# Kernel tuning notes

Measured on AMD Instinct MI355X. Metric: run time of the kernel, lower is better.

Reference implementation:

```python
import jax, jax.numpy as jnp
import numpy as np

EPS = 1e-06

def setup_inputs() -> dict:
    key = jax.random.key(0)
    k1, k2, k3, k4, k5 = jax.random.split(key, 5)
    B, T, D, Dv = 4, 2048, 128, 128
    q = jax.random.normal(k1, (B, T, D), dtype=jnp.float32)
    k = jax.random.normal(k2, (B, T, D), dtype=jnp.float32)
    v = jax.random.normal(k3, (B, T, Dv), dtype=jnp.float32)
    # phi = nn.Linear(dim, dim) followed by ELU; torch Linear default init ~ U(-1/sqrt(D), 1/sqrt(D))
    lim = 1.0 / np.sqrt(D)
    W_phi = jax.random.uniform(k4, (D, D), minval=-lim, maxval=lim, dtype=jnp.float32)
    b_phi = jax.random.uniform(k5, (D,), minval=-lim, maxval=lim, dtype=jnp.float32)
    return {"q": q, "k": k, "v": v, "W_phi": W_phi, "b_phi": b_phi}

def reference(q, k, v, W_phi, b_phi):
    # feature map: phi(x) = ELU(x @ W^T + b) + 1  (positive features)
    def phi(x):
        return jax.nn.elu(jnp.einsum('btd,ed->bte', x, W_phi) + b_phi) + 1.0

    Q = phi(q)                      # [B,T,D]
    K = phi(k)                      # [B,T,D]
    # causal recurrent state (zero initial state since h=None):
    # z_t = sum_{tau<=t} K_tau                 -> [B,T,D]
    # s_t = sum_{tau<=t} K_tau (outer) v_tau   -> [B,T,D,Dv]
    z = jnp.cumsum(K, axis=1)
    s = jnp.cumsum(K[..., :, None] * v[..., None, :], axis=1)
    den = jnp.einsum('btd,btd->bt', Q, z) + EPS          # [B,T]
    out = jnp.einsum('btd,btde->bte', Q, s) / den[..., None]  # [B,T,Dv]
    return out
```

## Files before the change

### kernel.cpp

```cpp
#include <hip/hip_runtime.h>
#include <hip/hip_bf16.h>

#define BB 4
#define TT 2048
#define DD 128
#define CHK 64
#define NCHK 32
#define NCHKS (BB*NCHK)

typedef __attribute__((ext_vector_type(8))) short  bf16x8;
typedef __attribute__((ext_vector_type(4))) float  f32x4;

#define MFMA(a,b,c) __builtin_amdgcn_mfma_f32_16x16x32_bf16(a, b, c, 0, 0, 0)

__device__ __forceinline__ short f2b(float f) {
    union { float f; unsigned u; } x; x.f = f;
    unsigned r = x.u + 0x7fffu + ((x.u >> 16) & 1u);
    return (short)(r >> 16);
}
__device__ __forceinline__ float b2f(short s) {
    union { unsigned u; float f; } x; x.u = ((unsigned)(unsigned short)s) << 16;
    return x.f;
}
__device__ __forceinline__ bf16x8 cvt8(const float* p) {
    float4 a = *(const float4*)p, b = *(const float4*)(p + 4);
    bf16x8 r;
    r[0]=f2b(a.x); r[1]=f2b(a.y); r[2]=f2b(a.z); r[3]=f2b(a.w);
    r[4]=f2b(b.x); r[5]=f2b(b.y); r[6]=f2b(b.z); r[7]=f2b(b.w);
    return r;
}

__device__ __forceinline__ void w_to_lds(const float* __restrict__ W,
                                         short (*Wl)[DD + 8], int tid) {
    #pragma unroll
    for (int it = 0; it < 16; ++it) {
        int i = tid + it * 256;
        int row = i >> 5, c4 = (i & 31) * 4;
        float4 v = *(const float4*)(W + (size_t)row * DD + c4);
        unsigned lo = (unsigned short)f2b(v.x) | ((unsigned)(unsigned short)f2b(v.y) << 16);
        unsigned hi = (unsigned short)f2b(v.z) | ((unsigned)(unsigned short)f2b(v.w) << 16);
        uint2 p; p.x = lo; p.y = hi;
        *(uint2*)&Wl[row][c4] = p;
    }
}

__global__ __launch_bounds__(256) void k1_chunk(const float* __restrict__ kin,
                                                const float* __restrict__ vin,
                                                const float* __restrict__ W,
                                                const float* __restrict__ bias,
                                                short* __restrict__ Ss_g,
                                                float* __restrict__ zc_g,
                                                short* __restrict__ vT_g,
                                                short* __restrict__ Kf_g) {
    int c = blockIdx.x >> 1, h = blockIdx.x & 1;
    const float* kc = kin + (size_t)c * CHK * DD;
    const float* vc = vin + (size_t)c * CHK * DD;

    __shared__ __align__(16) short Wl  [DD][DD + 8];
    __shared__ __align__(16) short KfT [DD][CHK + 8];
    __shared__ __align__(16) short vT  [CHK][CHK + 8];
    __shared__ __align__(16) short stage[CHK][DD + 8];

    int tid = threadIdx.x, lane = tid & 63, w = tid >> 6;
    int l15 = lane & 15, l4 = lane >> 4;
    const f32x4 z4 = {0.f, 0.f, 0.f, 0.f};

    bf16x8 afk[4];
    {
        int row = 16 * w + l15;
        #pragma unroll
        for (int kk = 0; kk < 4; ++kk) afk[kk] = cvt8(kc + row * DD + kk * 32 + l4 * 8);
    }
    w_to_lds(W, Wl, tid);
    #pragma unroll
    for (int it = 0; it < 4; ++it) {
        int i = tid + it * 256;
        int t = i >> 4, c4 = (i & 15) * 4;
        float4 vv = *(const float4*)(vc + t * DD + 64 * h + c4);
        vT[c4 + 0][t] = f2b(vv.x); vT[c4 + 1][t] = f2b(vv.y);
        vT[c4 + 2][t] = f2b(vv.z); vT[c4 + 3][t] = f2b(vv.w);
    }
    __syncthreads();

    #pragma unroll
    for (int n = 0; n < 8; ++n) {
        int e = 16 * n + l15;
        f32x4 d = z4;
        #pragma unroll
        for (int kk = 0; kk < 4; ++kk) {
            bf16x8 bw = *(const bf16x8*)&Wl[e][kk * 32 + l4 * 8];
            d = MFMA(afk[kk], bw, d);
        }
        float bv = bias[e];
        #pragma unroll
        for (int j = 0; j < 4; ++j) {
            float zv = d[j] + bv;
            short r = f2b((zv > 0.f) ? (zv + 1.f) : __expf(zv));
            int t = 16 * w + l4 * 4 + j;
            KfT[e][t] = r;
            if (h == 0) stage[t][e] = r;
        }
    }
    __syncthreads();

    if (h == 0) {
        short* dst = Kf_g + (size_t)c * CHK * DD;
        #pragma unroll
        for (int it = 0; it < 4; ++it) {
            int i = tid + it * 256;
            int t = i >> 4, u = (i & 15) * 8;
            *(bf16x8*)(dst + t * DD + u) = *(const bf16x8*)&stage[t][u];
        }
        if (tid < DD) {
            float s = 0.f;
            #pragma unroll
            for (int t8 = 0; t8 < CHK / 8; ++t8) {
                bf16x8 kv = *(const bf16x8*)&KfT[tid][t8 * 8];
                #pragma unroll
                for (int j = 0; j < 8; ++j) s += b2f(kv[j]);
            }
            zc_g[(size_t)c * DD + tid] = s;
        }
    }
    #pragma unroll
    for (int it = 0; it < 2; ++it) {
        int i = tid + it * 256;
        int e = i >> 3, t0 = (i & 7) * 8;
        *(bf16x8*)(vT_g + (size_t)c * DD * CHK + (64 * h + e) * CHK + t0) =
            *(const bf16x8*)&vT[e][t0];
    }

    f32x4 sacc[2][4];
    #pragma unroll
    for (int mi = 0; mi < 2; ++mi)
        #pragma unroll
        for (int n = 0; n < 4; ++n) sacc[mi][n] = z4;
    #pragma unroll
    for (int kk = 0; kk < 2; ++kk) {
        bf16x8 afr[2];
        #pragma unroll
        for (int mi = 0; mi < 2; ++mi)
            afr[mi] = *(const bf16x8*)&KfT[16 * (2 * w + mi) + l15][kk * 32 + l4 * 8];
        #pragma unroll
        for (int n = 0; n < 4; ++n) {
            bf16x8 bfr = *(const bf16x8*)&vT[16 * n + l15][kk * 32 + l4 * 8];
            sacc[0][n] = MFMA(afr[0], bfr, sacc[0][n]);
            sacc[1][n] = MFMA(afr[1], bfr, sacc[1][n]);
        }
    }
    __syncthreads();

    #pragma unroll
    for (int mi = 0; mi < 2; ++mi)
        #pragma unroll
        for (int n = 0; n < 4; ++n) {
            int e = 16 * n + l15;
            #pragma unroll
            for (int j = 0; j < 4; ++j)
                stage[e][16 * (2 * w + mi) + l4 * 4 + j] = f2b(sacc[mi][n][j]);
        }
    __syncthreads();

    short* dst = Ss_g + (size_t)c * DD * DD + (size_t)(64 * h) * DD;
    #pragma unroll
    for (int it = 0; it < 4; ++it) {
        int i = tid + it * 256;
        int e = i >> 4, u = (i & 15) * 8;
        *(bf16x8*)(dst + e * DD + u) = *(const bf16x8*)&stage[e][u];
    }
}

__global__ __launch_bounds__(128) void k2_scan(const short* __restrict__ Ss_g,
                                               const float* __restrict__ zc_g,
                                               short* __restrict__ Sp_g,
                                               float* __restrict__ zp_g) {
    int e = blockIdx.x & 127, b = blockIdx.x >> 7;
    int d = threadIdx.x;
    size_t base = ((size_t)(b * NCHK) * DD + e) * DD + d;
    const size_t stride = (size_t)DD * DD;

    float vals[NCHK];
    #pragma unroll
    for (int c2 = 0; c2 < NCHK; ++c2) vals[c2] = b2f(Ss_g[base + c2 * stride]);
    float run = 0.f;
    #pragma unroll
    for (int c2 = 0; c2 < NCHK; ++c2) {
        Sp_g[base + c2 * stride] = f2b(run);
        run += vals[c2];
    }
    if (e == 0) {
        float vz[NCHK];
        #pragma unroll
        for (int c2 = 0; c2 < NCHK; ++c2) vz[c2] = zc_g[(size_t)(b * NCHK + c2) * DD + d];
        float rz = 0.f;
        #pragma unroll
        for (int c2 = 0; c2 < NCHK; ++c2) {
            zp_g[(size_t)(b * NCHK + c2) * DD + d] = rz;
            rz += vz[c2];
        }
    }
}

__global__ __launch_bounds__(256) void k3_out(const float* __restrict__ q,
                                              const float* __restrict__ W,
                                              const float* __restrict__ bias,
                                              const short* __restrict__ Kf_g,
                                              const short* __restrict__ Sp_g,
                                              const float* __restrict__ zp_g,
                                              const short* __restrict__ vT_g,
                                              float* __restrict__ out) {
    int c = blockIdx.x >> 1, h = blockIdx.x & 1;

    __shared__ __align__(16) short Wl[DD][DD + 8];
    __shared__ __align__(16) short Qf[CHK][DD + 8];
    __shared__ __align__(16) short Kf[CHK][DD + 8];
    __shared__ __align__(16) short Ps[CHK][CHK + 8];
    __shared__ float zs[DD];
    __shared__ float den[CHK];

    int tid = threadIdx.x, lane = tid & 63, w = tid >> 6;
    int l15 = lane & 15, l4 = lane >> 4;
    const f32x4 z4 = {0.f, 0.f, 0.f, 0.f};

    if (tid < DD) zs[tid] = zp_g[(size_t)c * DD + tid];

    const float* qc = q + (size_t)c * CHK * DD;
    bf16x8 afq[4];
    {
        int row = 16 * w + l15;
        #pragma unroll
        for (int kk = 0; kk < 4; ++kk)
            afq[kk] = cvt8(qc + row * DD + kk * 32 + l4 * 8);
    }
    w_to_lds(W, Wl, tid);
    {
        const short* src = Kf_g + (size_t)c * CHK * DD;
        #pragma unroll
        for (int it = 0; it < 4; ++it) {
            int i = tid + it * 256;
            int t = i >> 4, u = (i & 15) * 8;
            *(bf16x8*)&Kf[t][u] = *(const bf16x8*)(src + t * DD + u);
        }
    }
    __syncthreads();

    #pragma unroll
    for (int n = 0; n < 8; ++n) {
        int e = 16 * n + l15;
        f32x4 dq = z4;
        #pragma unroll
        for (int kk = 0; kk < 4; ++kk) {
            bf16x8 bw = *(const bf16x8*)&Wl[e][kk * 32 + l4 * 8];
            dq = MFMA(afq[kk], bw, dq);
        }
        float bv = bias[e];
        #pragma unroll
        for (int j = 0; j < 4; ++j) {
            float zq = dq[j] + bv;
            Qf[16 * w + l4 * 4 + j][e] = f2b((zq > 0.f) ? (zq + 1.f) : __expf(zq));
        }
    }
    __syncthreads();

    bf16x8 aq[4];
    #pragma unroll
    for (int kk = 0; kk < 4; ++kk)
        aq[kk] = *(const bf16x8*)&Qf[16 * w + l15][kk * 32 + l4 * 8];
    #pragma unroll
    for (int n2 = 0; n2 < 4; ++n2) {
        f32x4 p = z4;
        #pragma unroll
        for (int kk = 0; kk < 4; ++kk) {
            bf16x8 bk = *(const bf16x8*)&Kf[16 * n2 + l15][kk * 32 + l4 * 8];
            p = MFMA(aq[kk], bk, p);
        }
        int t2 = 16 * n2 + l15;
        #pragma unroll
        for (int j = 0; j < 4; ++j) {
            int t = 16 * w + l4 * 4 + j;
            Ps[t][t2] = (t2 <= t) ? f2b(p[j]) : (short)0;
        }
    }
    __syncthreads();

    if (tid < CHK) {
        float s = 1e-6f;
        #pragma unroll
        for (int t8 = 0; t8 < CHK / 8; ++t8) {
            bf16x8 pv = *(const bf16x8*)&Ps[tid][t8 * 8];
            #pragma unroll
            for (int j = 0; j < 8; ++j) s += b2f(pv[j]);
        }
        #pragma unroll
        for (int d8 = 0; d8 < DD / 8; ++d8) {
            bf16x8 qv = *(const bf16x8*)&Qf[tid][d8 * 8];
            #pragma unroll
            for (int j = 0; j < 8; ++j) s += b2f(qv[j]) * zs[d8 * 8 + j];
        }
        den[tid] = s;
    }

    bf16x8 ap[2];
    #pragma unroll
    for (int kk = 0; kk < 2; ++kk)
        ap[kk] = *(const bf16x8*)&Ps[16 * w + l15][kk * 32 + l4 * 8];

    const short* Sp  = Sp_g + (size_t)c * DD * DD;
    const short* vTg = vT_g + (size_t)c * DD * CHK;
    f32x4 oacc[4];
    #pragma unroll
    for (int n = 0; n < 4; ++n) oacc[n] = z4;
    #pragma unroll
    for (int n = 0; n < 4; ++n) {
        int e = 64 * h + 16 * n + l15;
        #pragma unroll
        for (int kk = 0; kk < 4; ++kk) {
            bf16x8 bs = *(const bf16x8*)(Sp + e * DD + kk * 32 + l4 * 8);
            oacc[n] = MFMA(aq[kk], bs, oacc[n]);
        }
        #pragma unroll
        for (int kk = 0; kk < 2; ++kk) {
            bf16x8 bv = *(const bf16x8*)(vTg + e * CHK + kk * 32 + l4 * 8);
            oacc[n] = MFMA(ap[kk], bv, oacc[n]);
        }
    }
    __syncthreads();

    float* oc = out + (size_t)c * CHK * DD;
    float invs[4];
    #pragma unroll
    for (int j = 0; j < 4; ++j) invs[j] = 1.0f / den[16 * w + l4 * 4 + j];
    #pragma unroll
    for (int n = 0; n < 4; ++n) {
        int e = 64 * h + 16 * n + l15;
        #pragma unroll
        for (int j = 0; j < 4; ++j) {
            int t = 16 * w + l4 * 4 + j;
            oc[t * DD + e] = oacc[n][j] * invs[j];
        }
    }
}

extern "C" void kernel_launch(void* const* d_in, const int* in_sizes, int n_in,
                              void* d_out, int out_size, void* d_ws, size_t ws_size,
                              hipStream_t stream) {
    const float* q  = (const float*)d_in[0];
    const float* k  = (const float*)d_in[1];
    const float* v  = (const float*)d_in[2];
    const float* W  = (const float*)d_in[3];
    const float* bi = (const float*)d_in[4];
    float* out = (float*)d_out;

    float* zc_g = (float*)d_ws;
    float* zp_g = zc_g + (size_t)NCHKS * DD;
    short* Ss_g = (short*)(zp_g + (size_t)NCHKS * DD);
    short* Sp_g = Ss_g + (size_t)NCHKS * DD * DD;
    short* vT_g = Sp_g + (size_t)NCHKS * DD * DD;
    short* Kf_g = vT_g + (size_t)NCHKS * DD * CHK;

    k1_chunk<<<2 * NCHKS, 256, 0, stream>>>(k, v, W, bi, Ss_g, zc_g, vT_g, Kf_g);
    k2_scan<<<512, 128, 0, stream>>>(Ss_g, zc_g, Sp_g, zp_g);
    k3_out<<<2 * NCHKS, 256, 0, stream>>>(q, W, bi, Kf_g, Sp_g, zp_g, vT_g, out);
}
```

Measured before the change: 28.38 us.

## Compute Q feature map in chunk kernel and pass bf16 Qf to output kernel

Moves the phi(q) projection out of the output kernel into the first chunk kernel, where the h=1 block (previously idle for the feature store) computes Q features and writes them as bf16 to workspace. The output kernel then just loads precomputed Qf and Kf from global memory instead of reloading W into LDS and running its own projection. This cuts duplicated W staging across both h-halves in k3 and shrinks k3's LDS footprint. In exchange it adds an extra bf16 global write and read of Q features and more work for the h=1 blocks of k1.

After: 27.31 us. -3.8%, faster.

```diff
diff --git a/kernel.cpp b/kernel.cpp
--- a/kernel.cpp
+++ b/kernel.cpp
@@ -30,8 +30,40 @@
     return r;
 }
 
-__device__ __forceinline__ void w_to_lds(const float* __restrict__ W,
-                                         short (*Wl)[DD + 8], int tid) {
+__global__ __launch_bounds__(256) void k1_chunk(const float* __restrict__ q,
+                                                const float* __restrict__ kin,
+                                                const float* __restrict__ vin,
+                                                const float* __restrict__ W,
+                                                const float* __restrict__ bias,
+                                                short* __restrict__ Ss_g,
+                                                float* __restrict__ zc_g,
+                                                short* __restrict__ vT_g,
+                                                short* __restrict__ Qf_g,
+                                                short* __restrict__ Kf_g) {
+    int c = blockIdx.x >> 1, h = blockIdx.x & 1;
+    const float* qc = q   + (size_t)c * CHK * DD;
+    const float* kc = kin + (size_t)c * CHK * DD;
+    const float* vc = vin + (size_t)c * CHK * DD;
+
+    __shared__ __align__(16) short Wl  [DD][DD + 8];
+    __shared__ __align__(16) short KfT [DD][CHK + 8];
+    __shared__ __align__(16) short vT  [CHK][CHK + 8];
+    __shared__ __align__(16) short stage[CHK][DD + 8];
+
+    int tid = threadIdx.x, lane = tid & 63, w = tid >> 6;
+    int l15 = lane & 15, l4 = lane >> 4;
+    const f32x4 z4 = {0.f, 0.f, 0.f, 0.f};
+
+    bf16x8 afk[4], afq[4];
+    {
+        int row = 16 * w + l15;
+        #pragma unroll
+        for (int kk = 0; kk < 4; ++kk) afk[kk] = cvt8(kc + row * DD + kk * 32 + l4 * 8);
+        if (h) {
+            #pragma unroll
+            for (int kk = 0; kk < 4; ++kk) afq[kk] = cvt8(qc + row * DD + kk * 32 + l4 * 8);
+        }
+    }
     #pragma unroll
     for (int it = 0; it < 16; ++it) {
         int i = tid + it * 256;
@@ -42,36 +74,6 @@
         uint2 p; p.x = lo; p.y = hi;
         *(uint2*)&Wl[row][c4] = p;
     }
-}
-
-__global__ __launch_bounds__(256) void k1_chunk(const float* __restrict__ kin,
-                                                const float* __restrict__ vin,
-                                                const float* __restrict__ W,
-                                                const float* __restrict__ bias,
-                                                short* __restrict__ Ss_g,
-                                                float* __restrict__ zc_g,
-                                                short* __restrict__ vT_g,
-                                                short* __restrict__ Kf_g) {
-    int c = blockIdx.x >> 1, h = blockIdx.x & 1;
-    const float* kc = kin + (size_t)c * CHK * DD;
-    const float* vc = vin + (size_t)c * CHK * DD;
-
-    __shared__ __align__(16) short Wl  [DD][DD + 8];
-    __shared__ __align__(16) short KfT [DD][CHK + 8];
-    __shared__ __align__(16) short vT  [CHK][CHK + 8];
-    __shared__ __align__(16) short stage[CHK][DD + 8];
-
-    int tid = threadIdx.x, lane = tid & 63, w = tid >> 6;
-    int l15 = lane & 15, l4 = lane >> 4;
-    const f32x4 z4 = {0.f, 0.f, 0.f, 0.f};
-
-    bf16x8 afk[4];
-    {
-        int row = 16 * w + l15;
-        #pragma unroll
-        for (int kk = 0; kk < 4; ++kk) afk[kk] = cvt8(kc + row * DD + kk * 32 + l4 * 8);
-    }
-    w_to_lds(W, Wl, tid);
     #pragma unroll
     for (int it = 0; it < 4; ++it) {
         int i = tid + it * 256;
@@ -101,26 +103,44 @@
             if (h == 0) stage[t][e] = r;
         }
     }
-    __syncthreads();
-
-    if (h == 0) {
-        short* dst = Kf_g + (size_t)c * CHK * DD;
+    if (h) {
+        #pragma unroll
+        for (int n = 0; n < 8; ++n) {
+            int e = 16 * n + l15;
+            f32x4 d = z4;
+            #pragma unroll
+            for (int kk = 0; kk < 4; ++kk) {
+                bf16x8 bw = *(const bf16x8*)&Wl[e][kk * 32 + l4 * 8];
+                d = MFMA(afq[kk], bw, d);
+            }
+            float bv = bias[e];
+            #pragma unroll
+            for (int j = 0; j < 4; ++j) {
+                float zv = d[j] + bv;
+                stage[16 * w + l4 * 4 + j][e] = f2b((zv > 0.f) ? (zv + 1.f) : __expf(zv));
+            }
+        }
+    }
+    __syncthreads();
+
+    {
+        short* dst = (h ? Qf_g : Kf_g) + (size_t)c * CHK * DD;
         #pragma unroll
         for (int it = 0; it < 4; ++it) {
             int i = tid + it * 256;
             int t = i >> 4, u = (i & 15) * 8;
             *(bf16x8*)(dst + t * DD + u) = *(const bf16x8*)&stage[t][u];
         }
-        if (tid < DD) {
-            float s = 0.f;
-            #pragma unroll
-            for (int t8 = 0; t8 < CHK / 8; ++t8) {
-                bf16x8 kv = *(const bf16x8*)&KfT[tid][t8 * 8];
-                #pragma unroll
-                for (int j = 0; j < 8; ++j) s += b2f(kv[j]);
-            }
-            zc_g[(size_t)c * DD + tid] = s;
-        }
+    }
+    if (h == 0 && tid < DD) {
+        float s = 0.f;
+        #pragma unroll
+        for (int t8 = 0; t8 < CHK / 8; ++t8) {
+            bf16x8 kv = *(const bf16x8*)&KfT[tid][t8 * 8];
+            #pragma unroll
+            for (int j = 0; j < 8; ++j) s += b2f(kv[j]);
+        }
+        zc_g[(size_t)c * DD + tid] = s;
     }
     #pragma unroll
     for (int it = 0; it < 2; ++it) {
@@ -201,9 +221,7 @@
     }
 }
 
-__global__ __launch_bounds__(256) void k3_out(const float* __restrict__ q,
-                                              const float* __restrict__ W,
-                                              const float* __restrict__ bias,
+__global__ __launch_bounds__(256) void k3_out(const short* __restrict__ Qf_g,
                                               const short* __restrict__ Kf_g,
                                               const short* __restrict__ Sp_g,
                                               const float* __restrict__ zp_g,
@@ -211,7 +229,6 @@
                                               float* __restrict__ out) {
     int c = blockIdx.x >> 1, h = blockIdx.x & 1;
 
-    __shared__ __align__(16) short Wl[DD][DD + 8];
     __shared__ __align__(16) short Qf[CHK][DD + 8];
     __shared__ __align__(16) short Kf[CHK][DD + 8];
     __shared__ __align__(16) short Ps[CHK][CHK + 8];
@@ -224,40 +241,15 @@
 
     if (tid < DD) zs[tid] = zp_g[(size_t)c * DD + tid];
 
-    const float* qc = q + (size_t)c * CHK * DD;
-    bf16x8 afq[4];
     {
-        int row = 16 * w + l15;
-        #pragma unroll
-        for (int kk = 0; kk < 4; ++kk)
-            afq[kk] = cvt8(qc + row * DD + kk * 32 + l4 * 8);
-    }
-    w_to_lds(W, Wl, tid);
-    {
-        const short* src = Kf_g + (size_t)c * CHK * DD;
+        const short* srcq = Qf_g + (size_t)c * CHK * DD;
+        const short* srck = Kf_g + (size_t)c * CHK * DD;
         #pragma unroll
         for (int it = 0; it < 4; ++it) {
             int i = tid + it * 256;
             int t = i >> 4, u = (i & 15) * 8;
-            *(bf16x8*)&Kf[t][u] = *(const bf16x8*)(src + t * DD + u);
-        }
-    }
-    __syncthreads();
-
-    #pragma unroll
-    for (int n = 0; n < 8; ++n) {
-        int e = 16 * n + l15;
-        f32x4 dq = z4;
-        #pragma unroll
-        for (int kk = 0; kk < 4; ++kk) {
-            bf16x8 bw = *(const bf16x8*)&Wl[e][kk * 32 + l4 * 8];
-            dq = MFMA(afq[kk], bw, dq);
-        }
-        float bv = bias[e];
-        #pragma unroll
-        for (int j = 0; j < 4; ++j) {
-            float zq = dq[j] + bv;
-            Qf[16 * w + l4 * 4 + j][e] = f2b((zq > 0.f) ? (zq + 1.f) : __expf(zq));
+            *(bf16x8*)&Qf[t][u] = *(const bf16x8*)(srcq + t * DD + u);
+            *(bf16x8*)&Kf[t][u] = *(const bf16x8*)(srck + t * DD + u);
         }
     }
     __syncthreads();
@@ -356,9 +348,10 @@
     short* Ss_g = (short*)(zp_g + (size_t)NCHKS * DD);
     short* Sp_g = Ss_g + (size_t)NCHKS * DD * DD;
     short* vT_g = Sp_g + (size_t)NCHKS * DD * DD;
-    short* Kf_g = vT_g + (size_t)NCHKS * DD * CHK;
-
-    k1_chunk<<<2 * NCHKS, 256, 0, stream>>>(k, v, W, bi, Ss_g, zc_g, vT_g, Kf_g);
+    short* Qf_g = vT_g + (size_t)NCHKS * DD * CHK;
+    short* Kf_g = Qf_g + (size_t)NCHKS * CHK * DD;
+
+    k1_chunk<<<2 * NCHKS, 256, 0, stream>>>(q, k, v, W, bi, Ss_g, zc_g, vT_g, Qf_g, Kf_g);
     k2_scan<<<512, 128, 0, stream>>>(Ss_g, zc_g, Sp_g, zp_g);
-    k3_out<<<2 * NCHKS, 256, 0, stream>>>(q, W, bi, Kf_g, Sp_g, zp_g, vT_g, out);
-}
+    k3_out<<<2 * NCHKS, 256, 0, stream>>>(Qf_g, Kf_g, Sp_g, zp_g, vT_g, out);
+}
```
